# Kernel tuning notes

Hardware: AMD Instinct MI355X
Metric: run time of the kernel (lower is better)

Reference implementation:

```python
import jax, jax.numpy as jnp
import numpy as np

R = 16
ALPHA = 32
SCALING = ALPHA / R  # 2.0
E = 8
TOP_K = 2


def setup_inputs() -> dict:
    key = jax.random.key(0)
    ks = jax.random.split(key, 5)
    B, S, D = 4, 2048, 4096
    x = jax.random.normal(ks[0], (B, S, D), dtype=jnp.float32)
    base_W = jax.random.normal(ks[1], (D, D), dtype=jnp.float32) * 0.02
    router_W = jax.random.normal(ks[2], (E, D), dtype=jnp.float32) * 0.02
    lora_A = jax.random.normal(ks[3], (E, D, R), dtype=jnp.float32) * 0.02
    lora_B = jax.random.normal(ks[4], (E, R, D), dtype=jnp.float32) * 0.02
    return {"x": x, "base_W": base_W, "router_W": router_W,
            "lora_A": lora_A, "lora_B": lora_B}


def reference(x, base_W, router_W, lora_A, lora_B):
    # base linear: y = x @ W^T  (nn.Linear, bias=False)
    base = jnp.einsum('bsd,od->bso', x, base_W)

    # router logits and top-2 routing (softmax in fp32, as in torch)
    logits = jnp.einsum('bsd,ed->bse', x, router_W)
    probs = jax.nn.softmax(logits.astype(jnp.float32), axis=-1)  # [B,S,E]
    top_vals, top_idx = jax.lax.top_k(probs, TOP_K)               # [B,S,2]
    rw = top_vals / jnp.sum(top_vals, axis=-1, keepdims=True)
    # scatter top-2 weights into dense [B,S,E] combine matrix
    w_dense = jnp.sum(jax.nn.one_hot(top_idx, E, dtype=rw.dtype) * rw[..., None],
                      axis=-2).astype(x.dtype)                    # [B,S,E]

    # expert LoRA: out_n = sum_e w_ne * (x_n @ A_e @ B_e)
    # apply routing weight at rank-r stage (B_e linear => same math),
    # avoiding the [B,S,E,D] intermediate.
    mid = jnp.einsum('bsd,edr->bser', x, lora_A)                  # [B,S,E,r]
    mid = mid * w_dense[..., None]
    inc = jnp.einsum('bser,erd->bsd', mid, lora_B)                # [B,S,D]

    return base + inc * SCALING
```

## Files before the change

kernel.cpp:

```cpp
#include <hip/hip_runtime.h>
#include <math.h>

#define DI __device__ __forceinline__

typedef __attribute__((ext_vector_type(4))) float  f32x4;
typedef __attribute__((ext_vector_type(4))) short  s16x4;
typedef __attribute__((ext_vector_type(8))) short  s16x8;
typedef __attribute__((ext_vector_type(4))) float  ffrag;
typedef s16x8 bfrag;

constexpr int NT = 8192;
constexpr int D  = 4096;
constexpr int NE = 8;
constexpr int KE = 128;
constexpr int KX = D + KE;

DI short f2bf(float f) {
  unsigned u = __builtin_bit_cast(unsigned, f);
  u += 0x7FFFu + ((u >> 16) & 1u);
  return (short)(u >> 16);
}
DI float bf2f(short h) {
  unsigned u = ((unsigned)(unsigned short)h) << 16;
  return __builtin_bit_cast(float, u);
}

#define GLOAD16(gp, lp)                                                        \
  __builtin_amdgcn_global_load_lds(                                            \
      (const __attribute__((address_space(1))) void*)(gp),                     \
      (__attribute__((address_space(3))) void*)(lp), 16, 0, 0)

__global__ void moe_k_detect(const unsigned* __restrict__ x, int* __restrict__ flag) {
  int l = threadIdx.x;
  int cnt = 0;
  for (int i = l; i < 2048; i += 64) {
    unsigned e = (x[i] >> 23) & 0xFFu;
    cnt += (e >= 110u && e <= 140u) ? 1 : 0;
  }
#pragma unroll
  for (int o = 32; o; o >>= 1) cnt += __shfl_xor(cnt, o);
  if (l == 0) flag[0] = (cnt > 1024) ? 0 : 1;
}

__global__ __launch_bounds__(256)
void moe_k_prep(const void* __restrict__ wp, const void* __restrict__ lAp,
                const void* __restrict__ lBp, const int* __restrict__ flag,
                short* __restrict__ Wb, short* __restrict__ Abt) {
  const bool bf = flag[0] != 0;
  int b = blockIdx.x, t = threadIdx.x;
  if (b < 8192) {
    int tid = b * 256 + t;
    int row = tid >> 9;
    int col = (tid & 511) << 3;
    s16x8 o;
    if (!bf) {
      const float* Wf = (const float*)wp;
      f32x4 v0 = *(const f32x4*)&Wf[(size_t)row * 4096 + col];
      f32x4 v1 = *(const f32x4*)&Wf[(size_t)row * 4096 + col + 4];
      o[0] = f2bf(v0[0]); o[1] = f2bf(v0[1]); o[2] = f2bf(v0[2]); o[3] = f2bf(v0[3]);
      o[4] = f2bf(v1[0]); o[5] = f2bf(v1[1]); o[6] = f2bf(v1[2]); o[7] = f2bf(v1[3]);
    } else {
      o = *(const s16x8*)&((const short*)wp)[(size_t)row * 4096 + col];
    }
    *(s16x8*)&Wb[(size_t)row * KX + col] = o;
  } else if (b < 8208) {
    int d = (b - 8192) * 256 + t;
    for (int j0 = 0; j0 < KE; j0 += 8) {
      s16x8 o;
#pragma unroll
      for (int i = 0; i < 8; ++i) {
        float v = bf ? bf2f(((const short*)lBp)[(size_t)(j0 + i) * 4096 + d])
                     : ((const float*)lBp)[(size_t)(j0 + i) * 4096 + d];
        o[i] = f2bf(2.0f * v);
      }
      *(s16x8*)&Wb[(size_t)d * KX + 4096 + j0] = o;
    }
  } else {
    int j = b - 8208;
    int e = j >> 4, r = j & 15;
    for (int d = t; d < 4096; d += 256) {
      size_t src = ((size_t)e * 4096 + d) * 16 + r;
      short v = bf ? ((const short*)lAp)[src] : f2bf(((const float*)lAp)[src]);
      Abt[(size_t)j * 4096 + d] = v;
    }
  }
}

__global__ __launch_bounds__(256)
void moe_k_xrouter(const void* __restrict__ xp, const void* __restrict__ rp,
                   const int* __restrict__ flag, short* __restrict__ Xb,
                   float* __restrict__ wdense) {
  const bool bf = flag[0] != 0;
  int t = threadIdx.x, wv = t >> 6, l = t & 63;
  int n = blockIdx.x * 4 + wv;
  float acc[NE];
#pragma unroll
  for (int e = 0; e < NE; ++e) acc[e] = 0.f;
  const float* xf = (const float*)xp;
  const short* xh = (const short*)xp;
  const float* rf = (const float*)rp;
  const short* rh = (const short*)rp;
  for (int it = 0; it < 16; ++it) {
    int d = it * 256 + l * 4;
    float x0, x1, x2, x3;
    s16x4 xo;
    if (!bf) {
      f32x4 v = *(const f32x4*)&xf[(size_t)n * D + d];
      x0 = v[0]; x1 = v[1]; x2 = v[2]; x3 = v[3];
      xo[0] = f2bf(x0); xo[1] = f2bf(x1); xo[2] = f2bf(x2); xo[3] = f2bf(x3);
    } else {
      xo = *(const s16x4*)&xh[(size_t)n * D + d];
      x0 = bf2f(xo[0]); x1 = bf2f(xo[1]); x2 = bf2f(xo[2]); x3 = bf2f(xo[3]);
    }
    *(s16x4*)&Xb[(size_t)n * KX + d] = xo;
#pragma unroll
    for (int e = 0; e < NE; ++e) {
      if (!bf) {
        f32x4 w = *(const f32x4*)&rf[(size_t)e * D + d];
        acc[e] += x0 * w[0] + x1 * w[1] + x2 * w[2] + x3 * w[3];
      } else {
        s16x4 w = *(const s16x4*)&rh[(size_t)e * D + d];
        acc[e] += x0 * bf2f(w[0]) + x1 * bf2f(w[1]) + x2 * bf2f(w[2]) + x3 * bf2f(w[3]);
      }
    }
  }
#pragma unroll
  for (int e = 0; e < NE; ++e) {
#pragma unroll
    for (int o = 32; o; o >>= 1) acc[e] += __shfl_xor(acc[e], o);
  }
  float m = acc[0];
#pragma unroll
  for (int e = 1; e < NE; ++e) m = fmaxf(m, acc[e]);
  float p[NE];
#pragma unroll
  for (int e = 0; e < NE; ++e) p[e] = __expf(acc[e] - m);
  int i1 = 0; float v1 = p[0];
#pragma unroll
  for (int e = 1; e < NE; ++e) { if (p[e] > v1) { v1 = p[e]; i1 = e; } }
  int i2 = 0; float v2 = -1.f;
#pragma unroll
  for (int e = 0; e < NE; ++e) { if (e != i1 && p[e] > v2) { v2 = p[e]; i2 = e; } }
  float inv = 1.f / (v1 + v2);
  if (l < NE) {
    float w = (l == i1) ? v1 * inv : ((l == i2) ? v2 * inv : 0.f);
    wdense[(size_t)n * NE + l] = w;
  }
}

__global__ __launch_bounds__(256)
void moe_k_mid(const short* __restrict__ Xb, const short* __restrict__ Abt,
               const float* __restrict__ wdense, short* __restrict__ XbW) {
  __shared__ __align__(16) short As[32 * 32];
  __shared__ __align__(16) short Bs[128 * 32];
  int t = threadIdx.x, wv = t >> 6, l = t & 63;
  int m0 = blockIdx.x * 32;
  ffrag acc[2][2];
#pragma unroll
  for (int i = 0; i < 2; ++i)
#pragma unroll
    for (int j = 0; j < 2; ++j)
#pragma unroll
      for (int q = 0; q < 4; ++q) acc[i][j][q] = 0.f;
  const int r2 = t >> 2, k8 = (t & 3) * 8;
  for (int kt = 0; kt < 128; ++kt) {
    int k0 = kt * 32;
    if (wv < 2) GLOAD16(&Xb[(size_t)(m0 + r2) * KX + k0 + k8], &As[wv * 512]);
    GLOAD16(&Abt[(size_t)r2 * 4096 + k0 + k8], &Bs[wv * 512]);
    GLOAD16(&Abt[(size_t)(64 + r2) * 4096 + k0 + k8], &Bs[2048 + wv * 512]);
    __syncthreads();
    int lr = l & 15, lk = (l >> 4) * 8;
    bfrag a0 = *(const bfrag*)&As[lr * 32 + lk];
    bfrag a1 = *(const bfrag*)&As[(16 + lr) * 32 + lk];
    bfrag b0 = *(const bfrag*)&Bs[(wv * 32 + lr) * 32 + lk];
    bfrag b1 = *(const bfrag*)&Bs[(wv * 32 + 16 + lr) * 32 + lk];
    acc[0][0] = __builtin_amdgcn_mfma_f32_16x16x32_bf16(a0, b0, acc[0][0], 0, 0, 0);
    acc[0][1] = __builtin_amdgcn_mfma_f32_16x16x32_bf16(a0, b1, acc[0][1], 0, 0, 0);
    acc[1][0] = __builtin_amdgcn_mfma_f32_16x16x32_bf16(a1, b0, acc[1][0], 0, 0, 0);
    acc[1][1] = __builtin_amdgcn_mfma_f32_16x16x32_bf16(a1, b1, acc[1][1], 0, 0, 0);
    __syncthreads();
  }
#pragma unroll
  for (int mm = 0; mm < 2; ++mm)
#pragma unroll
    for (int nn = 0; nn < 2; ++nn) {
      int e = wv * 2 + nn;
#pragma unroll
      for (int q = 0; q < 4; ++q) {
        int gr = m0 + mm * 16 + (l >> 4) * 4 + q;
        int j = wv * 32 + nn * 16 + (l & 15);
        float w = wdense[(size_t)gr * NE + e];
        XbW[(size_t)gr * KX + 4096 + j] = f2bf(acc[mm][nn][q] * w);
      }
    }
}

__global__ __launch_bounds__(512, 2)
void moe_k_main8(const short* __restrict__ Xb, const short* __restrict__ Wb,
                 const int* __restrict__ flag, void* __restrict__ outp) {
  __shared__ __align__(16) short LDS[65536];
  const int t = threadIdx.x;
  const int l = t & 63;
  const int wv = t >> 6;
  const int wr = wv >> 2;
  const int wc = wv & 3;
  const int lr = l & 15;
  const int kq = l >> 4;

  int wg = blockIdx.x;
  int swz = (wg & 7) * 64 + (wg >> 3);
  const int tm = (swz >> 4) * 256;
  const int tn = (swz & 15) * 256;

  ffrag acc[8][4];
#pragma unroll
  for (int i = 0; i < 8; ++i)
#pragma unroll
    for (int j = 0; j < 4; ++j)
#pragma unroll
      for (int q = 0; q < 4; ++q) acc[i][j][q] = 0.f;

#define STAGE_A(kt_)                                                           \
  do {                                                                         \
    int _k0 = (kt_) * 32, _b = ((kt_) & 3) * 16384;                            \
    _Pragma("unroll")                                                          \
    for (int _i = 0; _i < 2; ++_i) {                                           \
      int _c = _i * 512 + t;                                                   \
      int _r = _c >> 2;                                                        \
      int _kc = (_c & 3) ^ ((_r >> 1) & 3);                                    \
      GLOAD16(&Xb[(size_t)(tm + _r) * KX + _k0 + _kc * 8], &LDS[_b + _c * 8]); \
    }                                                                          \
  } while (0)
#define STAGE_B(kt_)                                                           \
  do {                                                                         \
    int _k0 = (kt_) * 32, _b = ((kt_) & 3) * 16384 + 8192;                     \
    _Pragma("unroll")                                                          \
    for (int _i = 0; _i < 2; ++_i) {                                           \
      int _c = _i * 512 + t;                                                   \
      int _r = _c >> 2;                                                        \
      int _kc = (_c & 3) ^ ((_r >> 1) & 3);                                    \
      GLOAD16(&Wb[(size_t)(tn + _r) * KX + _k0 + _kc * 8], &LDS[_b + _c * 8]); \
    }                                                                          \
  } while (0)

  STAGE_A(0); STAGE_B(0);
  STAGE_A(1); STAGE_B(1);
  STAGE_A(2); STAGE_B(2);

  constexpr int NKT = KX / 32;

  const int kx = kq ^ ((lr >> 1) & 3);
  const int aofs = (wr * 128 + lr) * 32 + kx * 8;
  const int bofs = 8192 + (wc * 64 + lr) * 32 + kx * 8;

#define MFMA_ROW(mi, av)                                                           \
  acc[mi][0] = __builtin_amdgcn_mfma_f32_16x16x32_bf16(av, b0, acc[mi][0], 0, 0, 0); \
  acc[mi][1] = __builtin_amdgcn_mfma_f32_16x16x32_bf16(av, b1, acc[mi][1], 0, 0, 0); \
  acc[mi][2] = __builtin_amdgcn_mfma_f32_16x16x32_bf16(av, b2, acc[mi][2], 0, 0, 0); \
  acc[mi][3] = __builtin_amdgcn_mfma_f32_16x16x32_bf16(av, b3, acc[mi][3], 0, 0, 0);

  for (int kt = 0; kt < NKT; ++kt) {
    if (kt + 2 < NKT)      asm volatile("s_waitcnt vmcnt(8)" ::: "memory");
    else if (kt + 1 < NKT) asm volatile("s_waitcnt vmcnt(4)" ::: "memory");
    else                   asm volatile("s_waitcnt vmcnt(0)" ::: "memory");
    __builtin_amdgcn_s_barrier();
    asm volatile("" ::: "memory");

    const int bufs = (kt & 3) * 16384;
    const short* Ab = &LDS[bufs + aofs];
    const short* Bb = &LDS[bufs + bofs];

    bfrag b0 = *(const bfrag*)&Bb[0];
    bfrag b1 = *(const bfrag*)&Bb[512];
    bfrag b2 = *(const bfrag*)&Bb[1024];
    bfrag b3 = *(const bfrag*)&Bb[1536];
    bfrag a0 = *(const bfrag*)&Ab[0];
    bfrag a1 = *(const bfrag*)&Ab[512];
    bfrag a2 = *(const bfrag*)&Ab[1024];
    bfrag a3 = *(const bfrag*)&Ab[1536];
    if (kt + 3 < NKT) STAGE_A(kt + 3);
    __builtin_amdgcn_s_setprio(1);
    MFMA_ROW(0, a0) MFMA_ROW(1, a1) MFMA_ROW(2, a2) MFMA_ROW(3, a3)
    __builtin_amdgcn_s_setprio(0);
    __builtin_amdgcn_s_barrier();
    asm volatile("" ::: "memory");

    bfrag a4 = *(const bfrag*)&Ab[2048];
    bfrag a5 = *(const bfrag*)&Ab[2560];
    bfrag a6 = *(const bfrag*)&Ab[3072];
    bfrag a7 = *(const bfrag*)&Ab[3584];
    if (kt + 3 < NKT) STAGE_B(kt + 3);
    __builtin_amdgcn_s_setprio(1);
    MFMA_ROW(4, a4) MFMA_ROW(5, a5) MFMA_ROW(6, a6) MFMA_ROW(7, a7)
    __builtin_amdgcn_s_setprio(0);
  }

  const bool bf = flag[0] != 0;
  float* of = (float*)outp;
  unsigned short* oh = (unsigned short*)outp;
#pragma unroll
  for (int m = 0; m < 8; ++m)
#pragma unroll
    for (int n = 0; n < 4; ++n)
#pragma unroll
      for (int q = 0; q < 4; ++q) {
        int gr = tm + wr * 128 + m * 16 + kq * 4 + q;
        int gc = tn + wc * 64 + n * 16 + lr;
        float v = acc[m][n][q];
        if (!bf) of[(size_t)gr * D + gc] = v;
        else     oh[(size_t)gr * D + gc] = (unsigned short)f2bf(v);
      }
#undef STAGE_A
#undef STAGE_B
#undef MFMA_ROW
}

extern "C" void kernel_launch(void* const* d_in, const int* in_sizes, int n_in,
                              void* d_out, int out_size, void* d_ws, size_t ws_size,
                              hipStream_t stream) {
  const void* x  = d_in[0];
  const void* bw = d_in[1];
  const void* rw = d_in[2];
  const void* lA = d_in[3];
  const void* lB = d_in[4];

  char* ws = (char*)d_ws;
  const size_t XB_BYTES  = (size_t)NT * KX * 2;
  const size_t WB_BYTES  = (size_t)D * KX * 2;
  const size_t ABT_BYTES = (size_t)KE * D * 2;
  const size_t WD_BYTES  = (size_t)NT * NE * 4;
  const size_t NEED = 256 + XB_BYTES + WB_BYTES + ABT_BYTES + WD_BYTES;
  if (ws_size < NEED) return;

  int*   flag   = (int*)ws;
  short* Xb     = (short*)(ws + 256);
  short* Wb     = (short*)(ws + 256 + XB_BYTES);
  short* Abt    = (short*)(ws + 256 + XB_BYTES + WB_BYTES);
  float* wdense = (float*)(ws + 256 + XB_BYTES + WB_BYTES + ABT_BYTES);

  hipLaunchKernelGGL(moe_k_detect, dim3(1), dim3(64), 0, stream,
                     (const unsigned*)x, flag);
  hipLaunchKernelGGL(moe_k_prep, dim3(8336), dim3(256), 0, stream,
                     bw, lA, lB, flag, Wb, Abt);
  hipLaunchKernelGGL(moe_k_xrouter, dim3(NT / 4), dim3(256), 0, stream,
                     x, rw, flag, Xb, wdense);
  hipLaunchKernelGGL(moe_k_mid, dim3(NT / 32), dim3(256), 0, stream,
                     Xb, Abt, wdense, Xb);
  hipLaunchKernelGGL(moe_k_main8, dim3(512), dim3(512), 0, stream,
                     Xb, Wb, flag, d_out);
}
```

Baseline: 429.1 us.

## Pipeline LoRA mid GEMM, swap MFMA operands for vectorized stores, move barriers

```diff
diff --git a/kernel.cpp b/kernel.cpp
--- a/kernel.cpp
+++ b/kernel.cpp
@@ -149,12 +149,15 @@
 }
 
 __global__ __launch_bounds__(256)
-void moe_k_mid(const short* __restrict__ Xb, const short* __restrict__ Abt,
-               const float* __restrict__ wdense, short* __restrict__ XbW) {
-  __shared__ __align__(16) short As[32 * 32];
-  __shared__ __align__(16) short Bs[128 * 32];
-  int t = threadIdx.x, wv = t >> 6, l = t & 63;
-  int m0 = blockIdx.x * 32;
+void moe_k_mid2(const short* __restrict__ Xb, const short* __restrict__ Abt,
+                const float* __restrict__ wdense, short* __restrict__ XbW) {
+  __shared__ __align__(16) short LDS[16384];
+  const int t = threadIdx.x, l = t & 63, wv = t >> 6;
+  const int wr = wv >> 1, wc = wv & 1;
+  const int lr = l & 15, kq = l >> 4;
+  const int m0 = (blockIdx.x >> 1) * 64;
+  const int j0 = (blockIdx.x & 1) * 64;
+
   ffrag acc[2][2];
 #pragma unroll
   for (int i = 0; i < 2; ++i)
@@ -162,37 +165,55 @@
     for (int j = 0; j < 2; ++j)
 #pragma unroll
       for (int q = 0; q < 4; ++q) acc[i][j][q] = 0.f;
-  const int r2 = t >> 2, k8 = (t & 3) * 8;
-  for (int kt = 0; kt < 128; ++kt) {
-    int k0 = kt * 32;
-    if (wv < 2) GLOAD16(&Xb[(size_t)(m0 + r2) * KX + k0 + k8], &As[wv * 512]);
-    GLOAD16(&Abt[(size_t)r2 * 4096 + k0 + k8], &Bs[wv * 512]);
-    GLOAD16(&Abt[(size_t)(64 + r2) * 4096 + k0 + k8], &Bs[2048 + wv * 512]);
-    __syncthreads();
-    int lr = l & 15, lk = (l >> 4) * 8;
-    bfrag a0 = *(const bfrag*)&As[lr * 32 + lk];
-    bfrag a1 = *(const bfrag*)&As[(16 + lr) * 32 + lk];
-    bfrag b0 = *(const bfrag*)&Bs[(wv * 32 + lr) * 32 + lk];
-    bfrag b1 = *(const bfrag*)&Bs[(wv * 32 + 16 + lr) * 32 + lk];
-    acc[0][0] = __builtin_amdgcn_mfma_f32_16x16x32_bf16(a0, b0, acc[0][0], 0, 0, 0);
-    acc[0][1] = __builtin_amdgcn_mfma_f32_16x16x32_bf16(a0, b1, acc[0][1], 0, 0, 0);
-    acc[1][0] = __builtin_amdgcn_mfma_f32_16x16x32_bf16(a1, b0, acc[1][0], 0, 0, 0);
-    acc[1][1] = __builtin_amdgcn_mfma_f32_16x16x32_bf16(a1, b1, acc[1][1], 0, 0, 0);
-    __syncthreads();
-  }
-#pragma unroll
-  for (int mm = 0; mm < 2; ++mm)
-#pragma unroll
-    for (int nn = 0; nn < 2; ++nn) {
-      int e = wv * 2 + nn;
-#pragma unroll
-      for (int q = 0; q < 4; ++q) {
-        int gr = m0 + mm * 16 + (l >> 4) * 4 + q;
-        int j = wv * 32 + nn * 16 + (l & 15);
-        float w = wdense[(size_t)gr * NE + e];
-        XbW[(size_t)gr * KX + 4096 + j] = f2bf(acc[mm][nn][q] * w);
-      }
-    }
+
+  const int srow = t >> 2, sslot = t & 3;
+#define MSTAGE(kt_)                                                            \
+  do {                                                                         \
+    int _k0 = (kt_) * 32, _b = ((kt_) & 3) * 4096;                             \
+    GLOAD16(&Xb[(size_t)(m0 + srow) * KX + _k0 + sslot * 8], &LDS[_b + t * 8]);\
+    GLOAD16(&Abt[(size_t)(j0 + srow) * 4096 + _k0 + sslot * 8],                \
+            &LDS[_b + 2048 + t * 8]);                                          \
+  } while (0)
+
+  MSTAGE(0); MSTAGE(1); MSTAGE(2);
+  constexpr int NKT = 128;
+
+  for (int kt = 0; kt < NKT; ++kt) {
+    if (kt + 2 < NKT)      asm volatile("s_waitcnt vmcnt(4)" ::: "memory");
+    else if (kt + 1 < NKT) asm volatile("s_waitcnt vmcnt(2)" ::: "memory");
+    else                   asm volatile("s_waitcnt vmcnt(0)" ::: "memory");
+    __builtin_amdgcn_s_barrier();
+    __builtin_amdgcn_sched_barrier(0);
+
+    const int bufs = (kt & 3) * 4096;
+    const short* As = &LDS[bufs + (wr * 32 + lr) * 32 + kq * 8];
+    const short* Bs = &LDS[bufs + 2048 + (wc * 32 + lr) * 32 + kq * 8];
+    bfrag a0 = *(const bfrag*)&As[0];
+    bfrag a1 = *(const bfrag*)&As[512];
+    bfrag b0 = *(const bfrag*)&Bs[0];
+    bfrag b1 = *(const bfrag*)&Bs[512];
+    if (kt + 3 < NKT) MSTAGE(kt + 3);
+    asm volatile("" ::: "memory");
+    acc[0][0] = __builtin_amdgcn_mfma_f32_16x16x32_bf16(b0, a0, acc[0][0], 0, 0, 0);
+    acc[0][1] = __builtin_amdgcn_mfma_f32_16x16x32_bf16(b1, a0, acc[0][1], 0, 0, 0);
+    acc[1][0] = __builtin_amdgcn_mfma_f32_16x16x32_bf16(b0, a1, acc[1][0], 0, 0, 0);
+    acc[1][1] = __builtin_amdgcn_mfma_f32_16x16x32_bf16(b1, a1, acc[1][1], 0, 0, 0);
+  }
+
+#pragma unroll
+  for (int m = 0; m < 2; ++m)
+#pragma unroll
+    for (int n = 0; n < 2; ++n) {
+      int gr = m0 + wr * 32 + m * 16 + lr;
+      int jb = j0 + wc * 32 + n * 16 + kq * 4;
+      int e  = jb >> 4;
+      float w = wdense[(size_t)gr * NE + e];
+      s16x4 o;
+#pragma unroll
+      for (int q = 0; q < 4; ++q) o[q] = f2bf(acc[m][n][q] * w);
+      *(s16x4*)&XbW[(size_t)gr * KX + 4096 + jb] = o;
+    }
+#undef MSTAGE
 }
 
 __global__ __launch_bounds__(512, 2)
@@ -254,17 +275,17 @@
   const int bofs = 8192 + (wc * 64 + lr) * 32 + kx * 8;
 
 #define MFMA_ROW(mi, av)                                                           \
-  acc[mi][0] = __builtin_amdgcn_mfma_f32_16x16x32_bf16(av, b0, acc[mi][0], 0, 0, 0); \
-  acc[mi][1] = __builtin_amdgcn_mfma_f32_16x16x32_bf16(av, b1, acc[mi][1], 0, 0, 0); \
-  acc[mi][2] = __builtin_amdgcn_mfma_f32_16x16x32_bf16(av, b2, acc[mi][2], 0, 0, 0); \
-  acc[mi][3] = __builtin_amdgcn_mfma_f32_16x16x32_bf16(av, b3, acc[mi][3], 0, 0, 0);
+  acc[mi][0] = __builtin_amdgcn_mfma_f32_16x16x32_bf16(b0, av, acc[mi][0], 0, 0, 0); \
+  acc[mi][1] = __builtin_amdgcn_mfma_f32_16x16x32_bf16(b1, av, acc[mi][1], 0, 0, 0); \
+  acc[mi][2] = __builtin_amdgcn_mfma_f32_16x16x32_bf16(b2, av, acc[mi][2], 0, 0, 0); \
+  acc[mi][3] = __builtin_amdgcn_mfma_f32_16x16x32_bf16(b3, av, acc[mi][3], 0, 0, 0);
 
   for (int kt = 0; kt < NKT; ++kt) {
     if (kt + 2 < NKT)      asm volatile("s_waitcnt vmcnt(8)" ::: "memory");
     else if (kt + 1 < NKT) asm volatile("s_waitcnt vmcnt(4)" ::: "memory");
     else                   asm volatile("s_waitcnt vmcnt(0)" ::: "memory");
     __builtin_amdgcn_s_barrier();
-    asm volatile("" ::: "memory");
+    __builtin_amdgcn_sched_barrier(0);
 
     const int bufs = (kt & 3) * 16384;
     const short* Ab = &LDS[bufs + aofs];
@@ -279,17 +300,21 @@
     bfrag a2 = *(const bfrag*)&Ab[1024];
     bfrag a3 = *(const bfrag*)&Ab[1536];
     if (kt + 3 < NKT) STAGE_A(kt + 3);
+    asm volatile("" ::: "memory");
+    __builtin_amdgcn_s_barrier();
+    __builtin_amdgcn_sched_barrier(0);
     __builtin_amdgcn_s_setprio(1);
     MFMA_ROW(0, a0) MFMA_ROW(1, a1) MFMA_ROW(2, a2) MFMA_ROW(3, a3)
     __builtin_amdgcn_s_setprio(0);
-    __builtin_amdgcn_s_barrier();
-    asm volatile("" ::: "memory");
 
     bfrag a4 = *(const bfrag*)&Ab[2048];
     bfrag a5 = *(const bfrag*)&Ab[2560];
     bfrag a6 = *(const bfrag*)&Ab[3072];
     bfrag a7 = *(const bfrag*)&Ab[3584];
     if (kt + 3 < NKT) STAGE_B(kt + 3);
+    asm volatile("" ::: "memory");
+    __builtin_amdgcn_s_barrier();
+    __builtin_amdgcn_sched_barrier(0);
     __builtin_amdgcn_s_setprio(1);
     MFMA_ROW(4, a4) MFMA_ROW(5, a5) MFMA_ROW(6, a6) MFMA_ROW(7, a7)
     __builtin_amdgcn_s_setprio(0);
@@ -301,15 +326,18 @@
 #pragma unroll
   for (int m = 0; m < 8; ++m)
 #pragma unroll
-    for (int n = 0; n < 4; ++n)
-#pragma unroll
-      for (int q = 0; q < 4; ++q) {
-        int gr = tm + wr * 128 + m * 16 + kq * 4 + q;
-        int gc = tn + wc * 64 + n * 16 + lr;
-        float v = acc[m][n][q];
-        if (!bf) of[(size_t)gr * D + gc] = v;
-        else     oh[(size_t)gr * D + gc] = (unsigned short)f2bf(v);
+    for (int n = 0; n < 4; ++n) {
+      int gr = tm + wr * 128 + m * 16 + lr;
+      int gc = tn + wc * 64 + n * 16 + kq * 4;
+      if (!bf) {
+        *(f32x4*)&of[(size_t)gr * D + gc] = acc[m][n];
+      } else {
+        s16x4 o;
+#pragma unroll
+        for (int q = 0; q < 4; ++q) o[q] = f2bf(acc[m][n][q]);
+        *(s16x4*)&oh[(size_t)gr * D + gc] = o;
       }
+    }
 #undef STAGE_A
 #undef STAGE_B
 #undef MFMA_ROW
@@ -344,7 +372,7 @@
                      bw, lA, lB, flag, Wb, Abt);
   hipLaunchKernelGGL(moe_k_xrouter, dim3(NT / 4), dim3(256), 0, stream,
                      x, rw, flag, Xb, wdense);
-  hipLaunchKernelGGL(moe_k_mid, dim3(NT / 32), dim3(256), 0, stream,
+  hipLaunchKernelGGL(moe_k_mid2, dim3(256), dim3(256), 0, stream,
                      Xb, Abt, wdense, Xb);
   hipLaunchKernelGGL(moe_k_main8, dim3(512), dim3(512), 0, stream,
                      Xb, Wb, flag, d_out);
```

Measured after the change: 403.7 us. -5.9%, faster.
